# Performance work log

Hardware: AMD Instinct MI355X
Metric: run time of the kernel (lower is better)

Reference implementation:

```python
import jax, jax.numpy as jnp
import numpy as np
from functools import partial

B, S, D, H, DK, DV, DFF = 4, 2048, 1024, 8, 128, 128, 4096
EPS = 1e-6

def rms_norm(x):
    return x * jax.lax.rsqrt(jnp.mean(x * x, axis=-1, keepdims=True) + EPS)

def l2norm(x):
    return x * jax.lax.rsqrt(jnp.sum(x * x, axis=-1, keepdims=True) + EPS)

def setup_inputs() -> dict:
    key = jax.random.key(0)
    ks = jax.random.split(key, 16)
    w = lambda k, shp: jax.random.normal(k, shp, dtype=jnp.float32) * 0.02
    return {
        'x': jax.random.normal(ks[0], (B, S, D), dtype=jnp.float32),
        'Wq': w(ks[1], (D, H * DK)),
        'Wk': w(ks[2], (D, H * DK)),
        'Wv': w(ks[3], (D, H * DV)),
        'Wb': w(ks[4], (D, H)),
        'Wa': w(ks[5], (D, H)),
        'A_log': jnp.log(jnp.linspace(1.0, 8.0, H).astype(jnp.float32)),
        'dt_bias': jax.random.normal(ks[6], (H,), dtype=jnp.float32) * 0.1,
        'Wg': w(ks[7], (D, H * DV)),
        'o_norm_w': jnp.ones((DV,), dtype=jnp.float32),
        'Wo': w(ks[8], (H * DV, D)),
        'W_fc': w(ks[9], (D, DFF)),
        'W_proj': w(ks[10], (DFF, D)),
    }

def gated_delta_net(h, Wq, Wk, Wv, Wb, Wa, A_log, dt_bias, Wg, o_norm_w, Wo):
    b, s, _ = h.shape
    q = l2norm(jax.nn.silu(h @ Wq).reshape(b, s, H, DK))
    k = l2norm(jax.nn.silu(h @ Wk).reshape(b, s, H, DK))
    v = jax.nn.silu(h @ Wv).reshape(b, s, H, DV)
    beta = jax.nn.sigmoid(h @ Wb)                                  # [b,s,H]
    g = -jnp.exp(A_log) * jax.nn.softplus(h @ Wa + dt_bias)       # [b,s,H]
    alpha = jnp.exp(g)
    scale = DK ** -0.5

    # time-major for scan
    tm = lambda a: jnp.moveaxis(a, 1, 0)
    qs, ks_, vs, als, bts = tm(q), tm(k), tm(v), tm(alpha), tm(beta)

    def step(Sst, inp):
        q_t, k_t, v_t, a_t, b_t = inp               # [b,H,dk],[b,H,dk],[b,H,dv],[b,H],[b,H]
        Sst = Sst * a_t[..., None, None]            # decay state [b,H,dk,dv]
        kv = jnp.einsum('bhd,bhde->bhe', k_t, Sst)  # current memory readout
        delta = (v_t - kv) * b_t[..., None]
        Sst = Sst + jnp.einsum('bhd,bhe->bhde', k_t, delta)
        o_t = jnp.einsum('bhd,bhde->bhe', q_t, Sst) * scale
        return Sst, o_t

    S0 = jnp.zeros((b, H, DK, DV), dtype=h.dtype)
    _, o = jax.lax.scan(step, S0, (qs, ks_, vs, als, bts))
    o = jnp.moveaxis(o, 0, 1)                       # [b,s,H,dv]

    gate = (h @ Wg).reshape(b, s, H, DV)
    o = rms_norm(o) * o_norm_w * jax.nn.silu(gate)  # gated RMSNorm
    return o.reshape(b, s, H * DV) @ Wo

def reference(x, Wq, Wk, Wv, Wb, Wa, A_log, dt_bias, Wg, o_norm_w, Wo, W_fc, W_proj):
    ln_scale = 1.0  # config.layer_norm_scaling = False
    h = gated_delta_net(ln_scale * rms_norm(x), Wq, Wk, Wv, Wb, Wa, A_log, dt_bias, Wg, o_norm_w, Wo)
    x = x + h
    m = ln_scale * rms_norm(x)
    y = jnp.square(jax.nn.relu(m @ W_fc)) @ W_proj  # nanoGPT ReLU^2 MLP
    return x + y
```

## Files before the change

### kernel.cpp

```cpp
#include <hip/hip_runtime.h>
#include <math.h>
#include <stdint.h>

#define ROWS 8192
#define DIM  1024
#define NH   8
#define DFF_ 4096
#define EPSF 1e-6f
#define SCALEQ 0.08838834764831845f

typedef __attribute__((ext_vector_type(8))) short short8;
typedef __attribute__((ext_vector_type(4))) float f32x4;

__device__ __forceinline__ float siluf(float x) {
    return x / (1.0f + expf(-x));
}
__device__ __forceinline__ unsigned short f2bf(float f) {
    uint32_t u = __float_as_uint(f);
    uint32_t r = (u + 0x7FFFu + ((u >> 16) & 1u)) >> 16;
    return (unsigned short)r;
}
__device__ __forceinline__ float bf2f(unsigned short u) {
    return __uint_as_float(((uint32_t)u) << 16);
}

__device__ __forceinline__ void async16(const void* g, void* l) {
    __builtin_amdgcn_global_load_lds(
        (const __attribute__((address_space(1))) uint32_t*)g,
        (__attribute__((address_space(3))) uint32_t*)l, 16, 0, 0);
}

__global__ void rmsnorm_bf16_kernel(const float* __restrict__ x, unsigned short* __restrict__ y) {
    int row = blockIdx.x;
    int tid = threadIdx.x;
    const float4* x4 = (const float4*)(x + (size_t)row * DIM);
    float4 v = x4[tid];
    float ss = v.x * v.x + v.y * v.y + v.z * v.z + v.w * v.w;
#pragma unroll
    for (int m = 1; m < 64; m <<= 1) ss += __shfl_xor(ss, m, 64);
    __shared__ float wss[4];
    if ((tid & 63) == 0) wss[tid >> 6] = ss;
    __syncthreads();
    float tot = wss[0] + wss[1] + wss[2] + wss[3];
    float r = rsqrtf(tot * (1.0f / 1024.0f) + EPSF);
    ushort4 o;
    o.x = f2bf(v.x * r); o.y = f2bf(v.y * r); o.z = f2bf(v.z * r); o.w = f2bf(v.w * r);
    ((ushort4*)(y + (size_t)row * DIM))[tid] = o;
}

__global__ void transpose_bf16_kernel(const float* __restrict__ W, unsigned short* __restrict__ WT,
                                      int K, int N) {
    __shared__ float tile[32][33];
    int n0 = blockIdx.x * 32, k0 = blockIdx.y * 32;
    int tx = threadIdx.x & 31, ty = threadIdx.x >> 5;
#pragma unroll
    for (int r = 0; r < 32; r += 8)
        tile[ty + r][tx] = W[(size_t)(k0 + ty + r) * N + n0 + tx];
    __syncthreads();
#pragma unroll
    for (int r = 0; r < 32; r += 8)
        WT[(size_t)(n0 + ty + r) * K + k0 + tx] = f2bf(tile[tx][ty + r]);
}


#define G256_DECL \
    __shared__ __align__(16) unsigned short AL[2][2][256 * 32]; \
    __shared__ __align__(16) unsigned short BL[2][2][256 * 32]; \
    int tid = threadIdx.x; \
    int w = tid >> 6, lane = tid & 63; \
    int wm = w >> 2, wn = w & 3; \
    int lr = lane & 15; \
    int nwgx = gridDim.x; \
    int nwg = nwgx * gridDim.y; \
    int id = blockIdx.y * nwgx + blockIdx.x; \
    int cpx = nwg >> 3; \
    int nid = (id & 7) * cpx + (id >> 3); \
    int bxs = nid % nwgx, bys = nid / nwgx; \
    int bm = bys * 256, bn = bxs * 256; \
    int stg_r = w * 32 + (lane >> 2); \
    int stg_c = ((lane & 3) ^ ((lane >> 3) & 3)) * 8; \
    const unsigned short* Ag = A + (size_t)(bm + stg_r) * K + stg_c; \
    const unsigned short* Bg = BT + (size_t)(bn + stg_r) * K + stg_c; \
    int pc = ((lane >> 4) ^ ((lr >> 1) & 3)) * 8; \
    f32x4 acc[8][4] = {}; \
    short8 bf[4], af[4]; \
    int nt = K / 64;

#define G256_STAGE_A(buf, s, kto) do { \
    async16(Ag + (kto) + (s) * 32, &AL[buf][s][(w * 2 + 0) * 512]); \
    async16(Ag + (size_t)16 * K + (kto) + (s) * 32, &AL[buf][s][(w * 2 + 1) * 512]); \
} while (0)
#define G256_STAGE_B(buf, s, kto) do { \
    async16(Bg + (kto) + (s) * 32, &BL[buf][s][(w * 2 + 0) * 512]); \
    async16(Bg + (size_t)16 * K + (kto) + (s) * 32, &BL[buf][s][(w * 2 + 1) * 512]); \
} while (0)

#define G256_READ_B(cur, s) do { \
    _Pragma("unroll") \
    for (int j = 0; j < 4; ++j) \
        bf[j] = *(const short8*)&BL[cur][s][(wn * 64 + j * 16 + lr) * 32 + pc]; \
} while (0)
#define G256_READ_A(cur, s, rh) do { \
    _Pragma("unroll") \
    for (int i = 0; i < 4; ++i) \
        af[i] = *(const short8*)&AL[cur][s][(wm * 128 + (rh) * 64 + i * 16 + lr) * 32 + pc]; \
} while (0)

#define G256_MFMA(rh) do { \
    __builtin_amdgcn_s_barrier(); \
    asm volatile("s_waitcnt lgkmcnt(0)" ::: "memory"); \
    __builtin_amdgcn_s_setprio(1); \
    _Pragma("unroll") \
    for (int i = 0; i < 4; ++i) \
        _Pragma("unroll") \
        for (int j = 0; j < 4; ++j) \
            acc[(rh) * 4 + i][j] = __builtin_amdgcn_mfma_f32_16x16x32_bf16(af[i], bf[j], acc[(rh) * 4 + i][j], 0, 0, 0); \
    __builtin_amdgcn_s_setprio(0); \
} while (0)

#define G256_MAINLOOP \
    G256_STAGE_A(0, 0, 0); G256_STAGE_B(0, 0, 0); \
    G256_STAGE_A(0, 1, 0); G256_STAGE_B(0, 1, 0); \
    asm volatile("s_waitcnt vmcnt(0)" ::: "memory"); \
    __builtin_amdgcn_s_barrier(); \
    for (int t = 0; t < nt; ++t) { \
        int cur = t & 1, nxt = cur ^ 1; \
        bool pf = (t + 1 < nt); \
        int ktn = (t + 1) * 64; \
         \
        G256_READ_B(cur, 0); \
        G256_READ_A(cur, 0, 0); \
        if (pf) G256_STAGE_A(nxt, 0, ktn); \
        G256_MFMA(0); \
        __builtin_amdgcn_s_barrier(); \
         \
        G256_READ_A(cur, 0, 1); \
        if (pf) G256_STAGE_B(nxt, 0, ktn); \
        G256_MFMA(1); \
        asm volatile("s_waitcnt vmcnt(4)" ::: "memory"); \
        __builtin_amdgcn_s_barrier(); \
         \
        G256_READ_B(cur, 1); \
        G256_READ_A(cur, 1, 0); \
        if (pf) G256_STAGE_A(nxt, 1, ktn); \
        G256_MFMA(0); \
        __builtin_amdgcn_s_barrier(); \
         \
        G256_READ_A(cur, 1, 1); \
        if (pf) G256_STAGE_B(nxt, 1, ktn); \
        G256_MFMA(1); \
        asm volatile("s_waitcnt vmcnt(4)" ::: "memory"); \
        __builtin_amdgcn_s_barrier(); \
    }

template <int EPI, typename CT>
__global__ __launch_bounds__(512, 2) void gemm256(
    const unsigned short* __restrict__ A, const unsigned short* __restrict__ BT,
    CT* __restrict__ C, const float* __restrict__ res, int M, int N, int K) {
    G256_DECL
    G256_MAINLOOP

#pragma unroll
    for (int rf = 0; rf < 8; ++rf) {
        int gr0 = bm + wm * 128 + rf * 16 + (lane >> 4) * 4;
#pragma unroll
        for (int cf = 0; cf < 4; ++cf) {
            int gc = bn + wn * 64 + cf * 16 + lr;
#pragma unroll
            for (int r = 0; r < 4; ++r) {
                float v = acc[rf][cf][r];
                size_t idx = (size_t)(gr0 + r) * N + gc;
                if (EPI == 2) v += res[idx];
                else if (EPI == 3) { float t = fmaxf(v, 0.0f); v = t * t; }
                if constexpr (sizeof(CT) == 2) C[idx] = (CT)f2bf(v);
                else C[idx] = v;
            }
        }
    }
}

__global__ __launch_bounds__(512, 2) void qkvg256(
    const unsigned short* __restrict__ A, const unsigned short* __restrict__ BT,
    unsigned short* __restrict__ oq, unsigned short* __restrict__ ok,
    unsigned short* __restrict__ ov, unsigned short* __restrict__ og, int M, int K) {
    const int N = 4096;
    (void)N;
    __shared__ float sums[256 * 4];
    G256_DECL
    G256_MAINLOOP

    int bsel = bn >> 10;
    int bnl = bn & 1023;
    if (bsel < 3) {
#pragma unroll
        for (int rf = 0; rf < 8; ++rf)
#pragma unroll
            for (int cf = 0; cf < 4; ++cf)
#pragma unroll
                for (int r = 0; r < 4; ++r)
                    acc[rf][cf][r] = siluf(acc[rf][cf][r]);
    }
    bool donorm = (bsel < 2);
    if (donorm) {
#pragma unroll
        for (int rf = 0; rf < 8; ++rf) {
#pragma unroll
            for (int r = 0; r < 4; ++r) {
                float p = acc[rf][0][r] * acc[rf][0][r] + acc[rf][1][r] * acc[rf][1][r] +
                          acc[rf][2][r] * acc[rf][2][r] + acc[rf][3][r] * acc[rf][3][r];
                p += __shfl_xor(p, 1, 16);
                p += __shfl_xor(p, 2, 16);
                p += __shfl_xor(p, 4, 16);
                p += __shfl_xor(p, 8, 16);
                if (lr == 0)
                    sums[(wm * 128 + rf * 16 + (lane >> 4) * 4 + r) * 4 + wn] = p;
            }
        }
        __syncthreads();
    }
    unsigned short* C = (bsel == 0) ? oq : (bsel == 1) ? ok : (bsel == 2) ? ov : og;
#pragma unroll
    for (int rf = 0; rf < 8; ++rf) {
#pragma unroll
        for (int r = 0; r < 4; ++r) {
            int lrow = wm * 128 + rf * 16 + (lane >> 4) * 4 + r;
            float rn = 1.0f;
            if (donorm)
                rn = rsqrtf(sums[lrow * 4 + (wn & 2)] + sums[lrow * 4 + (wn & 2) + 1] + EPSF);
            size_t gr = (size_t)(bm + lrow) * 1024;
#pragma unroll
            for (int cf = 0; cf < 4; ++cf) {
                int gc = bnl + wn * 64 + cf * 16 + lr;
                C[gr + gc] = f2bf(acc[rf][cf][r] * rn);
            }
        }
    }
}

__global__ void gating_kernel(const float* __restrict__ o, const unsigned short* __restrict__ gate,
                              const float* __restrict__ w, unsigned short* __restrict__ ob) {
    int row = blockIdx.x;
    int tid = threadIdx.x;
    const float4* op = (const float4*)(o + (size_t)row * DIM);
    float4 v = op[tid];
    float ss = v.x * v.x + v.y * v.y + v.z * v.z + v.w * v.w;
#pragma unroll
    for (int m = 1; m < 32; m <<= 1) ss += __shfl_xor(ss, m, 32);
    float r = rsqrtf(ss * (1.0f / 128.0f) + EPSF);
    ushort4 gu = ((const ushort4*)(gate + (size_t)row * DIM))[tid];
    float4 wv = ((const float4*)w)[tid & 31];
    ushort4 out;
    out.x = f2bf(v.x * r * wv.x * siluf(bf2f(gu.x)));
    out.y = f2bf(v.y * r * wv.y * siluf(bf2f(gu.y)));
    out.z = f2bf(v.z * r * wv.z * siluf(bf2f(gu.z)));
    out.w = f2bf(v.w * r * wv.w * siluf(bf2f(gu.w)));
    ((ushort4*)(ob + (size_t)row * DIM))[tid] = out;
}

__global__ void smallproj_kernel(const unsigned short* __restrict__ hbuf,
                                 const float* __restrict__ Wb, const float* __restrict__ Wa,
                                 const float* __restrict__ A_log, const float* __restrict__ dt_bias,
                                 float* __restrict__ Glog, float* __restrict__ Beta) {
    int row = blockIdx.x;
    int tid = threadIdx.x;
    __shared__ __align__(16) float hrow[1024];
    __shared__ float part[128];
    const ushort4* h4 = (const ushort4*)(hbuf + (size_t)row * DIM);
    ushort4 u0 = h4[tid * 2], u1 = h4[tid * 2 + 1];
    hrow[tid * 8 + 0] = bf2f(u0.x); hrow[tid * 8 + 1] = bf2f(u0.y);
    hrow[tid * 8 + 2] = bf2f(u0.z); hrow[tid * 8 + 3] = bf2f(u0.w);
    hrow[tid * 8 + 4] = bf2f(u1.x); hrow[tid * 8 + 5] = bf2f(u1.y);
    hrow[tid * 8 + 6] = bf2f(u1.z); hrow[tid * 8 + 7] = bf2f(u1.w);
    __syncthreads();
    int out = tid & 15, slice = tid >> 4;
    const float* W = (out < 8) ? Wb : Wa;
    int col = out & 7;
    int k0 = slice * 128;
    float p = 0.0f;
    for (int kk = 0; kk < 128; kk++) p += hrow[k0 + kk] * W[(size_t)(k0 + kk) * 8 + col];
    part[tid] = p;
    __syncthreads();
    if (tid < 16) {
        float sum = 0.0f;
#pragma unroll
        for (int sl = 0; sl < 8; sl++) sum += part[sl * 16 + tid];
        if (tid < 8) {
            Beta[(size_t)row * 8 + tid] = 1.0f / (1.0f + expf(-sum));
        } else {
            int hh = tid - 8;
            float xg = sum + dt_bias[hh];
            float sp = fmaxf(xg, 0.0f) + log1pf(expf(-fabsf(xg)));
            Glog[(size_t)row * 8 + hh] = -expf(A_log[hh]) * sp;
        }
    }
}

#define PRE_KB 0
#define PRE_QB 17408
#define PRE_YL 17408
#define PRE_LM 34816
#define PRE_MT 44032
#define PRE_FL 76800
#define PRE_SZ 77824

__global__ __launch_bounds__(256) void chunk_prep_kernel(
    const unsigned short* __restrict__ Q16, const unsigned short* __restrict__ K16,
    const unsigned short* __restrict__ V16, const float* __restrict__ Glog,
    const float* __restrict__ Beta,
    unsigned short* __restrict__ Wg, unsigned short* __restrict__ Ug,
    unsigned short* __restrict__ Qg, unsigned short* __restrict__ KTg,
    unsigned short* __restrict__ SMg, float* __restrict__ Pcs) {
    __shared__ __align__(16) unsigned char smem[PRE_SZ];
    unsigned short* Kb = (unsigned short*)(smem + PRE_KB);
    unsigned short* Qb = (unsigned short*)(smem + PRE_QB);
    unsigned short* Yl = (unsigned short*)(smem + PRE_YL);
    unsigned short* Lm = (unsigned short*)(smem + PRE_LM);
    float* betl = (float*)(smem + PRE_FL);
    float* Gl = betl + 64;
    float* Pl = Gl + 64;
    float* decf = Pl + 64;

    int blk = blockIdx.x;
    int bh = blk & 31, c = blk >> 5;
    int b = bh >> 3, h = bh & 7;
    int bhc = bh * 32 + c;
    int row0 = b * 2048 + c * 64;
    int col0 = h * 128;
    int tid = threadIdx.x;
    int wv = tid >> 6, lane = tid & 63;
    int lr = lane & 15, lk8 = (lane >> 4) * 8, l4 = (lane >> 4) * 4;

#pragma unroll
    for (int r = 0; r < 4; ++r) {
        int cc = tid + r * 256;
        int i = cc >> 4, jc = (cc & 15) * 8;
        *(short8*)&Kb[i * 136 + jc] = *(const short8*)(K16 + (size_t)(row0 + i) * DIM + col0 + jc);
        *(short8*)&Qb[i * 136 + jc] = *(const short8*)(Q16 + (size_t)(row0 + i) * DIM + col0 + jc);
    }
    {
        short8 z = {};
        for (int o = tid; o < 576; o += 256) ((short8*)Lm)[o] = z;
        for (int o = tid; o < 2048; o += 256) ((short8*)(smem + PRE_MT))[o] = z;
    }
    if (tid < 64) {
        float g = Glog[(size_t)(row0 + tid) * 8 + h];
        betl[tid] = Beta[(size_t)(row0 + tid) * 8 + h];
#pragma unroll
        for (int d = 1; d < 64; d <<= 1) {
            float t = __shfl_up(g, d, 64);
            if (tid >= d) g += t;
        }
        Gl[tid] = g;
        Pl[tid] = expf(g);
        float g63 = __shfl(g, 63, 64);
        decf[tid] = expf(g63 - g);
        if (tid == 63) Pcs[bhc] = expf(g);
    }
    __syncthreads();

    for (int nt = 0; nt <= wv; nt++) {
        f32x4 acc = {};
#pragma unroll
        for (int kk = 0; kk < 4; kk++) {
            short8 af = *(const short8*)&Kb[(wv * 16 + lr) * 136 + kk * 32 + lk8];
            short8 bfr = *(const short8*)&Kb[(nt * 16 + lr) * 136 + kk * 32 + lk8];
            acc = __builtin_amdgcn_mfma_f32_16x16x32_bf16(af, bfr, acc, 0, 0, 0);
        }
#pragma unroll
        for (int r = 0; r < 4; r++) {
            int i = wv * 16 + l4 + r;
            int j = nt * 16 + lr;
            if (j < i) Lm[i * 72 + j] = f2bf(betl[i] * expf(Gl[i] - Gl[j]) * acc[r]);
        }
    }
    for (int nt = 0; nt < 4; nt++) {
        f32x4 acc = {};
        if (nt <= wv) {
#pragma unroll
            for (int kk = 0; kk < 4; kk++) {
                short8 af = *(const short8*)&Qb[(wv * 16 + lr) * 136 + kk * 32 + lk8];
                short8 bfr = *(const short8*)&Kb[(nt * 16 + lr) * 136 + kk * 32 + lk8];
                acc = __builtin_amdgcn_mfma_f32_16x16x32_bf16(af, bfr, acc, 0, 0, 0);
            }
        }
#pragma unroll
        for (int r = 0; r < 4; r++) {
            int i = wv * 16 + l4 + r;
            int j = nt * 16 + lr;
            float vv = (nt <= wv && j <= i) ? SCALEQ * expf(Gl[i] - Gl[j]) * acc[r] : 0.f;
            SMg[((size_t)bhc * 64 + i) * 64 + j] = f2bf(vv);
        }
    }
    {
        int d = tid & 127, ih = tid >> 7;
        for (int i0 = 0; i0 < 32; i0++) {
            int i = ih * 32 + i0;
            Qg[((size_t)bhc * 64 + i) * 128 + d] = f2bf(SCALEQ * Pl[i] * bf2f(Qb[i * 136 + d]));
        }
        for (int j8 = 0; j8 < 32; j8 += 8) {
            short8 v8;
#pragma unroll
            for (int e = 0; e < 8; e++) {
                int jj = ih * 32 + j8 + e;
                v8[e] = (short)f2bf(decf[jj] * bf2f(Kb[jj * 136 + d]));
            }
            *(short8*)&KTg[((size_t)bhc * 128 + d) * 64 + ih * 32 + j8] = v8;
        }
    }
    __syncthreads();

    int n = tid;
    bool isW = n < 128;
    int cW = n & 127;
    unsigned short* Gout = isW ? Wg : Ug;
    const unsigned short* Vcol = V16 + (size_t)row0 * DIM + col0 + cW;
    for (int bi = 0; bi < 4; ++bi) {
        if (bi > 0) {
            int ib = bi * 16;
#pragma unroll
            for (int t4 = 0; t4 < 4; ++t4) {
                int nt = wv * 4 + t4;
                f32x4 acc = {};
#pragma unroll
                for (int ks = 0; ks < 2; ++ks) {
                    short8 af = *(const short8*)&Lm[(ib + lr) * 72 + ks * 32 + lk8];
                    int nr = nt * 16 + lr;
                    int cj = ks * 4 + (lk8 >> 3);
                    short8 bfr = *(const short8*)(smem + PRE_MT + nr * 128 + (((cj ^ (nr & 7)) & 7) << 4));
                    acc = __builtin_amdgcn_mfma_f32_16x16x32_bf16(af, bfr, acc, 0, 0, 0);
                }
#pragma unroll
                for (int r = 0; r < 4; ++r)
                    Yl[(l4 + r) * 264 + nt * 16 + lr] = f2bf(acc[r]);
            }
        }
        __syncthreads();
        float xs[16];
#pragma unroll
        for (int ii = 0; ii < 16; ++ii) {
            int i = bi * 16 + ii;
            float a = isW ? betl[i] * Pl[i] * bf2f(Kb[i * 136 + cW])
                          : betl[i] * bf2f(Vcol[(size_t)i * DIM]);
            if (bi > 0) a -= bf2f(Yl[ii * 264 + n]);
#pragma unroll
            for (int j = 0; j < 15; ++j)
                if (j < ii) a = fmaf(-bf2f(Lm[i * 72 + bi * 16 + j]), xs[j], a);
            xs[ii] = a;
        }
        {
            short8 m0, m1;
#pragma unroll
            for (int e = 0; e < 8; ++e) { m0[e] = (short)f2bf(xs[e]); m1[e] = (short)f2bf(xs[8 + e]); }
            int cj0 = bi * 2, cj1 = bi * 2 + 1;
            *(short8*)(smem + PRE_MT + n * 128 + (((cj0 ^ (n & 7)) & 7) << 4)) = m0;
            *(short8*)(smem + PRE_MT + n * 128 + (((cj1 ^ (n & 7)) & 7) << 4)) = m1;
        }
#pragma unroll
        for (int ii = 0; ii < 16; ++ii)
            Gout[((size_t)bhc * 64 + bi * 16 + ii) * 128 + cW] = f2bf(xs[ii]);
        __syncthreads();
    }
}

__global__ __launch_bounds__(256) void chunk_scan2_kernel(
    const unsigned short* __restrict__ Wg, const unsigned short* __restrict__ Ug,
    const unsigned short* __restrict__ Qg, const unsigned short* __restrict__ KTg,
    const unsigned short* __restrict__ SMg, const float* __restrict__ Pcs,
    float* __restrict__ O) {
    int blk = blockIdx.x;
    int bh = blk & 31, dvg = blk >> 5;
    int b = bh >> 3, h = bh & 7;
    int col16 = dvg * 16;
    int tid = threadIdx.x;
    int wv = tid >> 6, lane = tid & 63;
    int lr = lane & 15, lk8 = (lane >> 4) * 8, l4 = (lane >> 4) * 4;
    int i0 = wv * 16;

    __shared__ __align__(16) unsigned short Wl[64 * 136];
    __shared__ __align__(16) unsigned short Ql[64 * 136];
    __shared__ __align__(16) unsigned short KTl[128 * 72];
    __shared__ __align__(16) unsigned short SMl[64 * 72];
    __shared__ __align__(16) unsigned short Ul[64 * 24];
    __shared__ __align__(16) unsigned short STl[16 * 136];
    __shared__ __align__(16) unsigned short DTl[16 * 72];

    for (int e = tid; e < 16 * 136; e += 256) STl[e] = 0;

    f32x4 Sacc[2] = {};

    for (int c = 0; c < 32; c++) {
        int bhc = bh * 32 + c;
        size_t base8k = (size_t)bhc * 8192;
        float pc = Pcs[bhc];
#pragma unroll
        for (int r = 0; r < 4; r++) {
            int v = tid + r * 256;
            *(short8*)&Wl[(v >> 4) * 136 + (v & 15) * 8] = *(const short8*)(Wg + base8k + (size_t)v * 8);
            *(short8*)&Ql[(v >> 4) * 136 + (v & 15) * 8] = *(const short8*)(Qg + base8k + (size_t)v * 8);
            *(short8*)&KTl[(v >> 3) * 72 + (v & 7) * 8] = *(const short8*)(KTg + base8k + (size_t)v * 8);
        }
#pragma unroll
        for (int r = 0; r < 2; r++) {
            int v = tid + r * 256;
            *(short8*)&SMl[(v >> 3) * 72 + (v & 7) * 8] = *(const short8*)(SMg + (size_t)bhc * 4096 + (size_t)v * 8);
        }
        if (tid < 128) {
            int row = tid >> 1, hf = tid & 1;
            *(short8*)&Ul[row * 24 + hf * 8] =
                *(const short8*)(Ug + base8k + (size_t)row * 128 + col16 + hf * 8);
        }
        __syncthreads();

        f32x4 acc0 = {}, acc1 = {};
#pragma unroll
        for (int kd = 0; kd < 4; kd++) {
            short8 bfs = *(const short8*)&STl[lr * 136 + kd * 32 + lk8];
            short8 aw = *(const short8*)&Wl[(i0 + lr) * 136 + kd * 32 + lk8];
            short8 aq = *(const short8*)&Ql[(i0 + lr) * 136 + kd * 32 + lk8];
            acc0 = __builtin_amdgcn_mfma_f32_16x16x32_bf16(aw, bfs, acc0, 0, 0, 0);
            acc1 = __builtin_amdgcn_mfma_f32_16x16x32_bf16(aq, bfs, acc1, 0, 0, 0);
        }
        ushort4 dpk;
        dpk.x = f2bf(bf2f(Ul[(i0 + l4 + 0) * 24 + lr]) - acc0[0]);
        dpk.y = f2bf(bf2f(Ul[(i0 + l4 + 1) * 24 + lr]) - acc0[1]);
        dpk.z = f2bf(bf2f(Ul[(i0 + l4 + 2) * 24 + lr]) - acc0[2]);
        dpk.w = f2bf(bf2f(Ul[(i0 + l4 + 3) * 24 + lr]) - acc0[3]);
        *(ushort4*)&DTl[lr * 72 + i0 + l4] = dpk;
        __syncthreads();

#pragma unroll
        for (int dt = 0; dt < 2; dt++)
#pragma unroll
            for (int r = 0; r < 4; r++) Sacc[dt][r] *= pc;
#pragma unroll
        for (int kj = 0; kj < 2; kj++) {
            short8 bfd = *(const short8*)&DTl[lr * 72 + kj * 32 + lk8];
            short8 as = *(const short8*)&SMl[(i0 + lr) * 72 + kj * 32 + lk8];
            acc1 = __builtin_amdgcn_mfma_f32_16x16x32_bf16(as, bfd, acc1, 0, 0, 0);
#pragma unroll
            for (int dt = 0; dt < 2; dt++) {
                short8 ak = *(const short8*)&KTl[((2 * wv + dt) * 16 + lr) * 72 + kj * 32 + lk8];
                Sacc[dt] = __builtin_amdgcn_mfma_f32_16x16x32_bf16(ak, bfd, Sacc[dt], 0, 0, 0);
            }
        }
        {
            int orow0 = b * 2048 + c * 64 + i0 + l4;
            int ocol = h * 128 + col16 + lr;
#pragma unroll
            for (int r = 0; r < 4; r++)
                O[(size_t)(orow0 + r) * DIM + ocol] = acc1[r];
        }
#pragma unroll
        for (int dt = 0; dt < 2; dt++) {
            ushort4 sp;
            sp.x = f2bf(Sacc[dt][0]);
            sp.y = f2bf(Sacc[dt][1]);
            sp.z = f2bf(Sacc[dt][2]);
            sp.w = f2bf(Sacc[dt][3]);
            *(ushort4*)&STl[lr * 136 + (2 * wv + dt) * 16 + l4] = sp;
        }
        __syncthreads();
    }
}

extern "C" void kernel_launch(void* const* d_in, const int* in_sizes, int n_in,
                              void* d_out, int out_size, void* d_ws, size_t ws_size,
                              hipStream_t stream) {
    const float* x      = (const float*)d_in[0];
    const float* Wq     = (const float*)d_in[1];
    const float* Wk     = (const float*)d_in[2];
    const float* Wv     = (const float*)d_in[3];
    const float* Wb     = (const float*)d_in[4];
    const float* Wa     = (const float*)d_in[5];
    const float* A_log  = (const float*)d_in[6];
    const float* dt_b   = (const float*)d_in[7];
    const float* Wg_in  = (const float*)d_in[8];
    const float* o_norm = (const float*)d_in[9];
    const float* Wo     = (const float*)d_in[10];
    const float* W_fc   = (const float*)d_in[11];
    const float* W_proj = (const float*)d_in[12];
    float* out = (float*)d_out;

    const size_t MATE = (size_t)ROWS * DIM;
    unsigned short* qb16 = (unsigned short*)d_ws;
    unsigned short* kb16 = qb16 + MATE;
    unsigned short* vb16 = kb16 + MATE;
    unsigned short* gt16 = vb16 + MATE;
    float* o_f = (float*)(gt16 + MATE);
    unsigned short* h_bf = (unsigned short*)(o_f + MATE);
    float* glog = (float*)(h_bf + MATE);
    float* beta = glog + (size_t)ROWS * NH;
    unsigned short* wts = (unsigned short*)(beta + (size_t)ROWS * NH);
    unsigned short* WqT = wts;
    unsigned short* WkT = wts + (1u << 20);
    unsigned short* WvT = wts + 2 * (1u << 20);
    unsigned short* WgT = wts + 3 * (1u << 20);
    unsigned short* WoT = wts + 4 * (1u << 20);
    unsigned short* WfcT = wts + 5 * (1u << 20);
    unsigned short* WprT = wts + 9 * (1u << 20);
    unsigned short* Wgb = wts + 13 * (1u << 20);
    unsigned short* Ugb = Wgb + (8u << 20);
    unsigned short* Qg2 = Ugb + (8u << 20);
    unsigned short* KTg = Qg2 + (8u << 20);
    unsigned short* SMg = KTg + (8u << 20);
    float* pcs = (float*)(SMg + (4u << 20));
    unsigned short* m_bf = h_bf;
    unsigned short* o_bf = vb16;
    unsigned short* fc_bf = qb16;

    transpose_bf16_kernel<<<dim3(32, 32), 256, 0, stream>>>(Wq, WqT, 1024, 1024);
    transpose_bf16_kernel<<<dim3(32, 32), 256, 0, stream>>>(Wk, WkT, 1024, 1024);
    transpose_bf16_kernel<<<dim3(32, 32), 256, 0, stream>>>(Wv, WvT, 1024, 1024);
    transpose_bf16_kernel<<<dim3(32, 32), 256, 0, stream>>>(Wg_in, WgT, 1024, 1024);
    transpose_bf16_kernel<<<dim3(32, 32), 256, 0, stream>>>(Wo, WoT, 1024, 1024);
    transpose_bf16_kernel<<<dim3(128, 32), 256, 0, stream>>>(W_fc, WfcT, 1024, 4096);
    transpose_bf16_kernel<<<dim3(32, 128), 256, 0, stream>>>(W_proj, WprT, 4096, 1024);

    rmsnorm_bf16_kernel<<<ROWS, 256, 0, stream>>>(x, h_bf);

    qkvg256<<<dim3(4096 / 256, ROWS / 256), 512, 0, stream>>>(
        h_bf, WqT, qb16, kb16, vb16, gt16, ROWS, DIM);

    smallproj_kernel<<<ROWS, 128, 0, stream>>>(h_bf, Wb, Wa, A_log, dt_b, glog, beta);

    chunk_prep_kernel<<<1024, 256, 0, stream>>>(qb16, kb16, vb16, glog, beta,
                                                Wgb, Ugb, Qg2, KTg, SMg, pcs);
    chunk_scan2_kernel<<<256, 256, 0, stream>>>(Wgb, Ugb, Qg2, KTg, SMg, pcs, o_f);

    gating_kernel<<<ROWS, 256, 0, stream>>>(o_f, gt16, o_norm, o_bf);

    gemm256<2, float><<<dim3(1024 / 256, ROWS / 256), 512, 0, stream>>>(
        o_bf, WoT, out, x, ROWS, DIM, DIM);

    rmsnorm_bf16_kernel<<<ROWS, 256, 0, stream>>>(out, m_bf);

    gemm256<3, unsigned short><<<dim3(DFF_ / 256, ROWS / 256), 512, 0, stream>>>(
        m_bf, WfcT, fc_bf, nullptr, ROWS, DFF_, DIM);

    gemm256<2, float><<<dim3(1024 / 256, ROWS / 256), 512, 0, stream>>>(
        fc_bf, WprT, out, out, ROWS, DIM, DFF_);
}
```

Baseline: 563.9 us.

## Use 128x256 tile GEMM for N=1024 projections to fill more CUs

Adds a GEMM kernel with 128x256 output tiles and a simplified two-stage LDS double-buffered pipeline. It replaces the 256x256 kernel for the Wo and W_proj projections, whose N=1024 output gave only 128 workgroups. Doubling the workgroup count aims to occupy all compute units. The cost is less operand reuse per tile and more global/LDS traffic per FLOP.

```diff
diff --git a/kernel.cpp b/kernel.cpp
--- a/kernel.cpp
+++ b/kernel.cpp
@@ -61,7 +61,6 @@
     for (int r = 0; r < 32; r += 8)
         WT[(size_t)(n0 + ty + r) * K + k0 + tx] = f2bf(tile[tx][ty + r]);
 }
-
 
 #define G256_DECL \
     __shared__ __align__(16) unsigned short AL[2][2][256 * 32]; \
@@ -127,25 +126,21 @@
         int cur = t & 1, nxt = cur ^ 1; \
         bool pf = (t + 1 < nt); \
         int ktn = (t + 1) * 64; \
-         \
         G256_READ_B(cur, 0); \
         G256_READ_A(cur, 0, 0); \
         if (pf) G256_STAGE_A(nxt, 0, ktn); \
         G256_MFMA(0); \
         __builtin_amdgcn_s_barrier(); \
-         \
         G256_READ_A(cur, 0, 1); \
         if (pf) G256_STAGE_B(nxt, 0, ktn); \
         G256_MFMA(1); \
         asm volatile("s_waitcnt vmcnt(4)" ::: "memory"); \
         __builtin_amdgcn_s_barrier(); \
-         \
         G256_READ_B(cur, 1); \
         G256_READ_A(cur, 1, 0); \
         if (pf) G256_STAGE_A(nxt, 1, ktn); \
         G256_MFMA(0); \
         __builtin_amdgcn_s_barrier(); \
-         \
         G256_READ_A(cur, 1, 1); \
         if (pf) G256_STAGE_B(nxt, 1, ktn); \
         G256_MFMA(1); \
@@ -183,8 +178,6 @@
     const unsigned short* __restrict__ A, const unsigned short* __restrict__ BT,
     unsigned short* __restrict__ oq, unsigned short* __restrict__ ok,
     unsigned short* __restrict__ ov, unsigned short* __restrict__ og, int M, int K) {
-    const int N = 4096;
-    (void)N;
     __shared__ float sums[256 * 4];
     G256_DECL
     G256_MAINLOOP
@@ -235,6 +228,99 @@
             }
         }
     }
+}
+
+template <int EPI>
+__global__ __launch_bounds__(512, 2) void gemm128n(
+    const unsigned short* __restrict__ A, const unsigned short* __restrict__ BT,
+    float* __restrict__ C, const float* __restrict__ res, int M, int N, int K) {
+    __shared__ __align__(16) unsigned short AL[2][2][128 * 32];
+    __shared__ __align__(16) unsigned short BL[2][2][256 * 32];
+    int tid = threadIdx.x;
+    int w = tid >> 6, lane = tid & 63;
+    int wm = w >> 2, wn = w & 3;
+    int lr = lane & 15;
+    int nwgx = gridDim.x;
+    int nwg = nwgx * gridDim.y;
+    int id = blockIdx.y * nwgx + blockIdx.x;
+    int cpx = nwg >> 3;
+    int nid = (id & 7) * cpx + (id >> 3);
+    int bxs = nid % nwgx, bys = nid / nwgx;
+    int bm = bys * 128, bn = bxs * 256;
+    int stg_r = w * 16 + (lane >> 2);
+    int stg_c = ((lane & 3) ^ ((lane >> 3) & 3)) * 8;
+    const unsigned short* Ag = A + (size_t)(bm + stg_r) * K + stg_c;
+    const unsigned short* Bg = BT + (size_t)(bn + stg_r) * K + stg_c;
+    int pc = ((lane >> 4) ^ ((lr >> 1) & 3)) * 8;
+    f32x4 acc[4][4] = {};
+    short8 bf[4], af[4];
+    int nt = K / 64;
+
+#define G128_STAGE_A(buf, s, kto) \
+    async16(Ag + (kto) + (s) * 32, &AL[buf][s][w * 512])
+#define G128_STAGE_B(buf, s, kto) do { \
+    async16(Bg + (kto) + (s) * 32, &BL[buf][s][w * 512]); \
+    async16(Bg + (size_t)128 * K + (kto) + (s) * 32, &BL[buf][s][4096 + w * 512]); \
+} while (0)
+#define G128_READ(cur, s) do { \
+    _Pragma("unroll") \
+    for (int j = 0; j < 4; ++j) \
+        bf[j] = *(const short8*)&BL[cur][s][(wn * 64 + j * 16 + lr) * 32 + pc]; \
+    _Pragma("unroll") \
+    for (int i = 0; i < 4; ++i) \
+        af[i] = *(const short8*)&AL[cur][s][(wm * 64 + i * 16 + lr) * 32 + pc]; \
+} while (0)
+#define G128_MFMA() do { \
+    __builtin_amdgcn_s_barrier(); \
+    asm volatile("s_waitcnt lgkmcnt(0)" ::: "memory"); \
+    __builtin_amdgcn_s_setprio(1); \
+    _Pragma("unroll") \
+    for (int i = 0; i < 4; ++i) \
+        _Pragma("unroll") \
+        for (int j = 0; j < 4; ++j) \
+            acc[i][j] = __builtin_amdgcn_mfma_f32_16x16x32_bf16(af[i], bf[j], acc[i][j], 0, 0, 0); \
+    __builtin_amdgcn_s_setprio(0); \
+} while (0)
+
+    G128_STAGE_A(0, 0, 0); G128_STAGE_B(0, 0, 0);
+    G128_STAGE_A(0, 1, 0); G128_STAGE_B(0, 1, 0);
+    asm volatile("s_waitcnt vmcnt(0)" ::: "memory");
+    __builtin_amdgcn_s_barrier();
+    for (int t = 0; t < nt; ++t) {
+        int cur = t & 1, nxt = cur ^ 1;
+        bool pf = (t + 1 < nt);
+        int ktn = (t + 1) * 64;
+        G128_READ(cur, 0);
+        if (pf) { G128_STAGE_A(nxt, 0, ktn); G128_STAGE_B(nxt, 0, ktn); }
+        G128_MFMA();
+        asm volatile("s_waitcnt vmcnt(3)" ::: "memory");
+        __builtin_amdgcn_s_barrier();
+        G128_READ(cur, 1);
+        if (pf) { G128_STAGE_A(nxt, 1, ktn); G128_STAGE_B(nxt, 1, ktn); }
+        G128_MFMA();
+        asm volatile("s_waitcnt vmcnt(3)" ::: "memory");
+        __builtin_amdgcn_s_barrier();
+    }
+
+#pragma unroll
+    for (int i = 0; i < 4; ++i) {
+        int gr0 = bm + wm * 64 + i * 16 + (lane >> 4) * 4;
+#pragma unroll
+        for (int j = 0; j < 4; ++j) {
+            int gc = bn + wn * 64 + j * 16 + lr;
+#pragma unroll
+            for (int r = 0; r < 4; ++r) {
+                float v = acc[i][j][r];
+                size_t idx = (size_t)(gr0 + r) * N + gc;
+                if (EPI == 2) v += res[idx];
+                C[idx] = v;
+            }
+        }
+    }
+#undef G128_STAGE_A
+#undef G128_STAGE_B
+#undef G128_READ
+#undef G128_MFMA
 }
 
 __global__ void gating_kernel(const float* __restrict__ o, const unsigned short* __restrict__ gate,
@@ -629,7 +715,7 @@
 
     gating_kernel<<<ROWS, 256, 0, stream>>>(o_f, gt16, o_norm, o_bf);
 
-    gemm256<2, float><<<dim3(1024 / 256, ROWS / 256), 512, 0, stream>>>(
+    gemm128n<2><<<dim3(1024 / 256, ROWS / 128), 512, 0, stream>>>(
         o_bf, WoT, out, x, ROWS, DIM, DIM);
 
     rmsnorm_bf16_kernel<<<ROWS, 256, 0, stream>>>(out, m_bf);
@@ -637,6 +723,6 @@
     gemm256<3, unsigned short><<<dim3(DFF_ / 256, ROWS / 256), 512, 0, stream>>>(
         m_bf, WfcT, fc_bf, nullptr, ROWS, DFF_, DIM);
 
-    gemm256<2, float><<<dim3(1024 / 256, ROWS / 256), 512, 0, stream>>>(
+    gemm128n<2><<<dim3(1024 / 256, ROWS / 128), 512, 0, stream>>>(
         fc_bf, WprT, out, out, ROWS, DIM, DFF_);
 }
```

Result: faster. 513.4 us (-8.9%).
